# Kernel optimization log

Measured on AMD Instinct MI355X. Metric: run time of the kernel, lower is better.

The kernel has to match this reference:

```python
import jax, jax.numpy as jnp
import numpy as np

B, N, D = 256, 131072, 256
TEMP = 0.05
EPS_SM = 1e-6
EPS_LOG = 1e-6
NUM_CLUSTERS = 1000


def _l2norm(x):
    return x / jnp.linalg.norm(x, axis=-1, keepdims=True)


def setup_inputs() -> dict:
    key = jax.random.key(0)
    k1, k2, k3, k4, k5 = jax.random.split(key, 5)
    # re-ID features are L2-normalized in practice; keeps exp(logits/temp) finite
    inputs = _l2norm(jax.random.normal(k1, (B, D), jnp.float32))
    indexes = jax.random.randint(k2, (B,), 0, N)
    labels = jax.random.randint(k3, (N,), 0, NUM_CLUSTERS)  # pseudo cluster ids buffer
    cluster_features = _l2norm(jax.random.normal(k4, (N, D), jnp.float32))
    instance_features = _l2norm(jax.random.normal(k5, (N, D), jnp.float32))
    return {
        "inputs": inputs,
        "cluster_features": cluster_features,
        "instance_features": instance_features,
        "indexes": indexes,
        "labels": labels,
    }


def reference(inputs, cluster_features, instance_features, indexes, labels):
    # targets = labels[indexes]
    targets = labels[indexes]
    # bank similarity GEMM, temperature scaling
    logits = jnp.matmul(inputs, cluster_features.T) / TEMP  # [B, N]
    # module's custom softmax: exp / (sum + eps)  (intentionally no max-subtract)
    exps = jnp.exp(logits)
    masked_sim = exps / (jnp.sum(exps, axis=1, keepdims=True) + EPS_SM)
    logp = jnp.log(masked_sim + EPS_LOG)
    # F.nll_loss: mean of -logp at target column
    loss = -jnp.mean(jnp.take_along_axis(logp, targets[:, None], axis=1))
    return loss
```

## Files before the change

kernel.cpp:

```cpp
#include <hip/hip_runtime.h>
#include <hip/hip_bf16.h>
#include <cstdint>

#define B_ 256
#define N_ 131072
#define D_ 256
#define INV_TEMP 20.0f
#define EPS_SM 1e-6f
#define EPS_LOG 1e-6f

#define TPB 512
#define BROWS 256
#define BN 64
#define BK 64
#define NCHUNK 16
#define LDB 72
#define BUFE (BN * LDB)
#define NSLOT 32
#define NBLK (N_ / BROWS)

typedef __bf16 bf16_t;
typedef bf16_t bf16x8 __attribute__((ext_vector_type(8)));
typedef float f32x4 __attribute__((ext_vector_type(4)));

struct alignas(16) U8 { ushort u[8]; };

__device__ inline ushort f2bf(float f) {
  return __builtin_bit_cast(ushort, (__bf16)f);
}

__device__ inline void cvt_store8(ushort* dst, const float4 a, const float4 b) {
  U8 w;
  w.u[0] = f2bf(a.x); w.u[1] = f2bf(a.y); w.u[2] = f2bf(a.z); w.u[3] = f2bf(a.w);
  w.u[4] = f2bf(b.x); w.u[5] = f2bf(b.y); w.u[6] = f2bf(b.z); w.u[7] = f2bf(b.w);
  *(uint4*)dst = __builtin_bit_cast(uint4, w);
}

__device__ inline void bar_ds() {
  asm volatile("s_waitcnt lgkmcnt(0)" ::: "memory");
  __builtin_amdgcn_s_barrier();
}

__global__ __launch_bounds__(TPB, 4)
void gemm_rowsum_fused(const float* __restrict__ inp, const float* __restrict__ cf,
                       const int* __restrict__ idx, const int* __restrict__ lab,
                       float* __restrict__ rowsum, unsigned* __restrict__ counter,
                       float* __restrict__ out) {
  __shared__ ushort smem[B_ * LDB];
  __shared__ unsigned done;
  const int tid  = threadIdx.x;
  const int wave = tid >> 6;
  const int lane = tid & 63;
  const int m15  = lane & 15;
  const int q    = lane >> 4;

  const size_t nbase = (size_t)blockIdx.x * BROWS;
  const int brow = tid >> 3, bcg = tid & 7;
#define LDADDR(c) (cf + (nbase + (size_t)((c) >> 2) * BN + brow) * D_ + ((c) & 3) * BK + bcg * 8)

  float4 ldbuf[2][2];
  ldbuf[0][0] = *(const float4*)(LDADDR(0));
  ldbuf[0][1] = *(const float4*)(LDADDR(0) + 4);
  ldbuf[1][0] = *(const float4*)(LDADDR(1));
  ldbuf[1][1] = *(const float4*)(LDADDR(1) + 4);

  bf16x8 areg[8][2];
#pragma unroll
  for (int kc = 0; kc < 4; ++kc) {
    const int row = tid >> 1, half = tid & 1;
    const float* src = inp + row * D_ + kc * BK + half * 32;
#pragma unroll
    for (int j = 0; j < 4; ++j) {
      const float4 v0 = *(const float4*)(src + j * 8);
      const float4 v1 = *(const float4*)(src + j * 8 + 4);
      cvt_store8(&smem[row * LDB + half * 32 + j * 8], v0, v1);
    }
    bar_ds();
#pragma unroll
    for (int mb = 0; mb < 2; ++mb)
#pragma unroll
      for (int ks = 0; ks < 2; ++ks)
        areg[kc * 2 + ks][mb] = __builtin_bit_cast(
            bf16x8, *(const uint4*)(&smem[(wave * 32 + mb * 16 + m15) * LDB + ks * 32 + q * 8]));
    bar_ds();
  }

  f32x4 acc[2][4];
  float rs[2][4];
#pragma unroll
  for (int mb = 0; mb < 2; ++mb) {
#pragma unroll
    for (int nb = 0; nb < 4; ++nb) acc[mb][nb] = (f32x4){0.f, 0.f, 0.f, 0.f};
#pragma unroll
    for (int r = 0; r < 4; ++r) rs[mb][r] = 0.f;
  }

  cvt_store8(&smem[brow * LDB + bcg * 8], ldbuf[0][0], ldbuf[0][1]);
  ldbuf[0][0] = *(const float4*)(LDADDR(2));
  ldbuf[0][1] = *(const float4*)(LDADDR(2) + 4);

#pragma unroll
  for (int c = 0; c < NCHUNK; ++c) {
    bar_ds();
    if (c + 1 < NCHUNK) {
      cvt_store8(&smem[((c + 1) & 1) * BUFE + brow * LDB + bcg * 8],
                 ldbuf[(c + 1) & 1][0], ldbuf[(c + 1) & 1][1]);
    }
    if (c + 3 < NCHUNK) {
      ldbuf[(c + 1) & 1][0] = *(const float4*)(LDADDR(c + 3));
      ldbuf[(c + 1) & 1][1] = *(const float4*)(LDADDR(c + 3) + 4);
    }
    const ushort* bs = &smem[(c & 1) * BUFE];
#pragma unroll
    for (int ks = 0; ks < 2; ++ks) {
      bf16x8 bfr[4];
#pragma unroll
      for (int nb = 0; nb < 4; ++nb)
        bfr[nb] = __builtin_bit_cast(
            bf16x8, *(const uint4*)(&bs[(nb * 16 + m15) * LDB + ks * 32 + q * 8]));
#pragma unroll
      for (int mb = 0; mb < 2; ++mb)
#pragma unroll
        for (int nb = 0; nb < 4; ++nb)
          acc[mb][nb] = __builtin_amdgcn_mfma_f32_16x16x32_bf16(
              areg[(c & 3) * 2 + ks][mb], bfr[nb], acc[mb][nb], 0, 0, 0);
    }
    if ((c & 3) == 3) {
#pragma unroll
      for (int mb = 0; mb < 2; ++mb)
#pragma unroll
        for (int nb = 0; nb < 4; ++nb)
#pragma unroll
          for (int r = 0; r < 4; ++r)
            rs[mb][r] += __expf(acc[mb][nb][r] * INV_TEMP);
      if (c + 1 < NCHUNK) {
#pragma unroll
        for (int mb = 0; mb < 2; ++mb)
#pragma unroll
          for (int nb = 0; nb < 4; ++nb) acc[mb][nb] = (f32x4){0.f, 0.f, 0.f, 0.f};
      }
    }
  }

#pragma unroll
  for (int off = 8; off >= 1; off >>= 1)
#pragma unroll
    for (int mb = 0; mb < 2; ++mb)
#pragma unroll
      for (int r = 0; r < 4; ++r)
        rs[mb][r] += __shfl_xor(rs[mb][r], off, 64);

  if (m15 == 0) {
    float* slot = rowsum + (blockIdx.x & (NSLOT - 1)) * B_;
#pragma unroll
    for (int mb = 0; mb < 2; ++mb)
#pragma unroll
      for (int r = 0; r < 4; ++r)
        atomicAdd(&slot[wave * 32 + mb * 16 + q * 4 + r], rs[mb][r]);
  }
#undef LDADDR

  __syncthreads();
  if (tid == 0) {
    __threadfence();
    const unsigned prev = __hip_atomic_fetch_add(counter, 1u, __ATOMIC_ACQ_REL,
                                                 __HIP_MEMORY_SCOPE_AGENT);
    done = (prev == (unsigned)(NBLK - 1)) ? 1u : 0u;
  }
  __syncthreads();
  if (done) {
    __threadfence();
    float* red = (float*)smem;
    const int b = tid >> 1, part = tid & 1;
    const int t = lab[idx[b]];
    const float4* a4 = (const float4*)(inp + b * D_ + part * 128);
    const float4* c4 = (const float4*)(cf + (size_t)t * D_ + part * 128);
    float dot = 0.f;
#pragma unroll
    for (int i = 0; i < 32; ++i) {
      const float4 x = a4[i], y = c4[i];
      dot += x.x * y.x + x.y * y.y + x.z * y.z + x.w * y.w;
    }
    red[tid] = dot;
    __syncthreads();
    if (tid < 256) {
      const float d = red[2 * tid] + red[2 * tid + 1];
      float S = 0.f;
#pragma unroll
      for (int s = 0; s < NSLOT; ++s)
        S += __hip_atomic_load(&rowsum[s * B_ + tid], __ATOMIC_RELAXED,
                               __HIP_MEMORY_SCOPE_AGENT);
      red[512 + tid] = __logf(__expf(d * INV_TEMP) / (S + EPS_SM) + EPS_LOG);
    }
    __syncthreads();
    for (int off = 128; off >= 1; off >>= 1) {
      if (tid < off) red[512 + tid] += red[512 + tid + off];
      __syncthreads();
    }
    if (tid == 0) out[0] = -red[512] * (1.0f / 256.0f);
  }
}

extern "C" void kernel_launch(void* const* d_in, const int* in_sizes, int n_in,
                              void* d_out, int out_size, void* d_ws, size_t ws_size,
                              hipStream_t stream) {
  const float* inp = (const float*)d_in[0];
  const float* cf  = (const float*)d_in[1];
  const int* idx = (const int*)d_in[3];
  const int* lab = (const int*)d_in[4];
  float* out = (float*)d_out;
  float* rowsum = (float*)d_ws;
  unsigned* counter = (unsigned*)(rowsum + NSLOT * B_);

  hipMemsetAsync(d_ws, 0, (NSLOT * B_ + 16) * sizeof(float), stream);
  gemm_rowsum_fused<<<dim3(NBLK), dim3(TPB), 0, stream>>>(inp, cf, idx, lab,
                                                          rowsum, counter, out);
}
```

Measured before the change: 337.1 us.

## Stream fp32 bank tiles directly to LDS with async loads and 4-slot ring

Replaces the register-staged global load, bf16 convert, LDS store path for cluster_features with global_load_lds DMA into a 4-buffer ring of fp32 tiles, staged two chunks ahead with XOR-swizzled addressing. The bf16 conversion now happens when fragments are read from LDS, and each chunk needs only one barrier. This is meant to cut VGPR pressure and instruction overhead on the load path and to hide more memory latency. In exchange, LDS traffic doubles because fp32 is stored, each fragment costs two 16-byte LDS reads plus conversion, and the LDS footprint grows to 64KB, which may reduce occupancy.

```diff
diff --git a/kernel.cpp b/kernel.cpp
--- a/kernel.cpp
+++ b/kernel.cpp
@@ -14,8 +14,10 @@
 #define BN 64
 #define BK 64
 #define NCHUNK 16
+#define CHUNK_B 16384
+#define NBUF 4
+#define A_OFF 28672
 #define LDB 72
-#define BUFE (BN * LDB)
 #define NSLOT 32
 #define NBLK (N_ / BROWS)
 
@@ -25,9 +27,7 @@
 
 struct alignas(16) U8 { ushort u[8]; };
 
-__device__ inline ushort f2bf(float f) {
-  return __builtin_bit_cast(ushort, (__bf16)f);
-}
+__device__ inline ushort f2bf(float f) { return __builtin_bit_cast(ushort, (__bf16)f); }
 
 __device__ inline void cvt_store8(ushort* dst, const float4 a, const float4 b) {
   U8 w;
@@ -36,9 +36,24 @@
   *(uint4*)dst = __builtin_bit_cast(uint4, w);
 }
 
+__device__ inline bf16x8 cvt_frag(const char* p) {
+  const float4 v0 = *(const float4*)p;
+  const float4 v1 = *(const float4*)(p + 16);
+  U8 w;
+  w.u[0] = f2bf(v0.x); w.u[1] = f2bf(v0.y); w.u[2] = f2bf(v0.z); w.u[3] = f2bf(v0.w);
+  w.u[4] = f2bf(v1.x); w.u[5] = f2bf(v1.y); w.u[6] = f2bf(v1.z); w.u[7] = f2bf(v1.w);
+  return __builtin_bit_cast(bf16x8, w);
+}
+
 __device__ inline void bar_ds() {
   asm volatile("s_waitcnt lgkmcnt(0)" ::: "memory");
   __builtin_amdgcn_s_barrier();
+}
+
+__device__ inline void load_lds16(const float* g, char* l) {
+  __builtin_amdgcn_global_load_lds(
+      (const __attribute__((address_space(1))) void*)g,
+      (__attribute__((address_space(3))) void*)l, 16, 0, 0);
 }
 
 __global__ __launch_bounds__(TPB, 4)
@@ -46,8 +61,9 @@
                        const int* __restrict__ idx, const int* __restrict__ lab,
                        float* __restrict__ rowsum, unsigned* __restrict__ counter,
                        float* __restrict__ out) {
-  __shared__ ushort smem[B_ * LDB];
+  __shared__ float4 smem4[4096];
   __shared__ unsigned done;
+  char* smem = (char*)smem4;
   const int tid  = threadIdx.x;
   const int wave = tid >> 6;
   const int lane = tid & 63;
@@ -55,15 +71,20 @@
   const int q    = lane >> 4;
 
   const size_t nbase = (size_t)blockIdx.x * BROWS;
-  const int brow = tid >> 3, bcg = tid & 7;
-#define LDADDR(c) (cf + (nbase + (size_t)((c) >> 2) * BN + brow) * D_ + ((c) & 3) * BK + bcg * 8)
-
-  float4 ldbuf[2][2];
-  ldbuf[0][0] = *(const float4*)(LDADDR(0));
-  ldbuf[0][1] = *(const float4*)(LDADDR(0) + 4);
-  ldbuf[1][0] = *(const float4*)(LDADDR(1));
-  ldbuf[1][1] = *(const float4*)(LDADDR(1) + 4);
-
+
+  const int srow = tid >> 4;
+  const int ssw  = (((tid & 15) * 16) ^ ((srow & 7) << 5)) >> 2;
+#define STAGE(c) do {                                                                  \
+    const float* g0 = cf + (nbase + (size_t)(((c) >> 2) * BN + srow)) * D_             \
+                         + ((c) & 3) * BK + ssw;                                       \
+    char* l0 = smem + ((c) & 3) * CHUNK_B + tid * 16;                                  \
+    load_lds16(g0, l0);                                                                \
+    load_lds16(g0 + 32 * D_, l0 + 8192);                                               \
+  } while (0)
+
+  STAGE(0);
+
+  ushort* asu = (ushort*)(smem + A_OFF);
   bf16x8 areg[8][2];
 #pragma unroll
   for (int kc = 0; kc < 4; ++kc) {
@@ -73,7 +94,7 @@
     for (int j = 0; j < 4; ++j) {
       const float4 v0 = *(const float4*)(src + j * 8);
       const float4 v1 = *(const float4*)(src + j * 8 + 4);
-      cvt_store8(&smem[row * LDB + half * 32 + j * 8], v0, v1);
+      cvt_store8(&asu[row * LDB + half * 32 + j * 8], v0, v1);
     }
     bar_ds();
 #pragma unroll
@@ -81,9 +102,11 @@
 #pragma unroll
       for (int ks = 0; ks < 2; ++ks)
         areg[kc * 2 + ks][mb] = __builtin_bit_cast(
-            bf16x8, *(const uint4*)(&smem[(wave * 32 + mb * 16 + m15) * LDB + ks * 32 + q * 8]));
+            bf16x8, *(const uint4*)(&asu[(wave * 32 + mb * 16 + m15) * LDB + ks * 32 + q * 8]));
     bar_ds();
   }
+
+  STAGE(1);
 
   f32x4 acc[2][4];
   float rs[2][4];
@@ -95,29 +118,30 @@
     for (int r = 0; r < 4; ++r) rs[mb][r] = 0.f;
   }
 
-  cvt_store8(&smem[brow * LDB + bcg * 8], ldbuf[0][0], ldbuf[0][1]);
-  ldbuf[0][0] = *(const float4*)(LDADDR(2));
-  ldbuf[0][1] = *(const float4*)(LDADDR(2) + 4);
+  const int sA = (m15 & 7) << 5;
+  const int t0 = (q * 32) ^ sA;
+  const int t1 = (128 + q * 32) ^ sA;
 
 #pragma unroll
   for (int c = 0; c < NCHUNK; ++c) {
-    bar_ds();
-    if (c + 1 < NCHUNK) {
-      cvt_store8(&smem[((c + 1) & 1) * BUFE + brow * LDB + bcg * 8],
-                 ldbuf[(c + 1) & 1][0], ldbuf[(c + 1) & 1][1]);
-    }
-    if (c + 3 < NCHUNK) {
-      ldbuf[(c + 1) & 1][0] = *(const float4*)(LDADDR(c + 3));
-      ldbuf[(c + 1) & 1][1] = *(const float4*)(LDADDR(c + 3) + 4);
-    }
-    const ushort* bs = &smem[(c & 1) * BUFE];
+    if (c + 2 < NCHUNK) STAGE(c + 2);
+    if (c < NCHUNK - 2) {
+      asm volatile("s_waitcnt vmcnt(4) lgkmcnt(0)" ::: "memory");
+    } else if (c == NCHUNK - 2) {
+      asm volatile("s_waitcnt vmcnt(2) lgkmcnt(0)" ::: "memory");
+    } else {
+      asm volatile("s_waitcnt vmcnt(0) lgkmcnt(0)" ::: "memory");
+    }
+    __builtin_amdgcn_s_barrier();
+    __builtin_amdgcn_sched_barrier(0);
+
+    const char* bs = smem + (c & 3) * CHUNK_B;
 #pragma unroll
     for (int ks = 0; ks < 2; ++ks) {
       bf16x8 bfr[4];
 #pragma unroll
       for (int nb = 0; nb < 4; ++nb)
-        bfr[nb] = __builtin_bit_cast(
-            bf16x8, *(const uint4*)(&bs[(nb * 16 + m15) * LDB + ks * 32 + q * 8]));
+        bfr[nb] = cvt_frag(bs + (nb * 16 + m15) * 256 + (ks ? t1 : t0));
 #pragma unroll
       for (int mb = 0; mb < 2; ++mb)
 #pragma unroll
@@ -141,6 +165,7 @@
       }
     }
   }
+#undef STAGE
 
 #pragma unroll
   for (int off = 8; off >= 1; off >>= 1)
@@ -158,7 +183,6 @@
       for (int r = 0; r < 4; ++r)
         atomicAdd(&slot[wave * 32 + mb * 16 + q * 4 + r], rs[mb][r]);
   }
-#undef LDADDR
 
   __syncthreads();
   if (tid == 0) {
```

After: 366.2 us. +8.6%, slower.
